# Kernel optimization log

Hardware: AMD Instinct MI355X
Metric: run time of the kernel (lower is better)

Reference implementation:

```python
import jax, jax.numpy as jnp
import numpy as np

N_NODES = 50000
IN_F, HID_F, OUT_F = 256, 128, 40
N_EDGES = 800000


def _uniform(key, shape, scale):
    return jax.random.uniform(key, shape, dtype=jnp.float32, minval=-scale, maxval=scale)


def setup_inputs() -> dict:
    key = jax.random.key(0)
    ks = jax.random.split(key, 20)
    x = jax.random.normal(ks[0], (N_NODES, IN_F), dtype=jnp.float32)
    edge_index = jax.random.randint(ks[1], (2, N_EDGES), 0, N_NODES, dtype=jnp.int64)
    s0, sa0 = 1.0 / np.sqrt(HID_F), 1.0  # std_att = 1/sqrt(1)
    s1, sa1 = 1.0 / np.sqrt(OUT_F), 1.0
    sv = 1.0 / np.sqrt(3.0)
    return {
        "x": x, "edge_index": edge_index,
        "Wl0": _uniform(ks[2], (IN_F, HID_F), s0),
        "Wh0": _uniform(ks[3], (IN_F, HID_F), s0),
        "Wm0": _uniform(ks[4], (IN_F, HID_F), s0),
        "al0": _uniform(ks[5], (HID_F, 1), sa0),
        "ah0": _uniform(ks[6], (HID_F, 1), sa0),
        "am0": _uniform(ks[7], (HID_F, 1), sa0),
        "att0": _uniform(ks[8], (3, 3), sv),
        "Wl1": _uniform(ks[9], (HID_F, OUT_F), s1),
        "Wh1": _uniform(ks[10], (HID_F, OUT_F), s1),
        "Wm1": _uniform(ks[11], (HID_F, OUT_F), s1),
        "al1": _uniform(ks[12], (OUT_F, 1), sa1),
        "ah1": _uniform(ks[13], (OUT_F, 1), sa1),
        "am1": _uniform(ks[14], (OUT_F, 1), sa1),
        "att1": _uniform(ks[15], (3, 3), sv),
    }


def _acm_layer(x, row, col, d_inv, Wl, Wh, Wm, al, ah, am, att):
    n = x.shape[0]
    hl, hh, hm = x @ Wl, x @ Wh, x @ Wm
    # adj_low @ M  with adj_low = D^{-1}(I + A): gather sources, scatter-add to rows
    def low(M):
        return d_inv[:, None] * (M + jax.ops.segment_sum(M[col], row, num_segments=n))
    out_low = jax.nn.relu(low(hl))
    out_high = jax.nn.relu(hh - low(hh))  # adj_high = I - adj_low
    out_mlp = jax.nn.relu(hm)
    T = 3.0
    sig = jax.nn.sigmoid(jnp.concatenate([out_low @ al, out_high @ ah, out_mlp @ am], axis=1))  # [n,3]
    a = jax.nn.softmax((sig @ att) / T, axis=1)
    return 3.0 * (a[:, 0:1] * out_low + a[:, 1:2] * out_high + a[:, 2:3] * out_mlp)


def reference(x, edge_index, Wl0, Wh0, Wm0, al0, ah0, am0, att0,
              Wl1, Wh1, Wm1, al1, ah1, am1, att1):
    n = x.shape[0]
    row, col = edge_index[0], edge_index[1]
    deg = jax.ops.segment_sum(jnp.ones_like(row, dtype=jnp.float32), row, num_segments=n)
    rowsum = 1.0 + deg  # rowsum of I + A (duplicates counted, as in scipy)
    d_inv = jnp.where(rowsum > 0, 1.0 / rowsum, 0.0)
    h = _acm_layer(x, row, col, d_inv, Wl0, Wh0, Wm0, al0, ah0, am0, att0)
    out = _acm_layer(h, row, col, d_inv, Wl1, Wh1, Wm1, al1, ah1, am1, att1)
    return out
```

## Files before the change

kernel.cpp:

```cpp
#include <hip/hip_runtime.h>
#include <math.h>

#define N_NODES 50000
#define N_EDGES 800000
#define IN_F    256
#define HID_F   128
#define OUT_F   40
#define W0N     (3*HID_F)
#define W1N     (3*OUT_F)
#define NB      ((N_NODES + 255) / 256)

#define XB   6250
#define P0B  ((IN_F * W0N) / 256)
#define P1B  ((HID_F * W1N) / 256)
#define CB0  (XB + P0B + P1B)
#define CNTB ((N_EDGES + 255) / 256)
#define PREPB (CB0 + CNTB)

typedef __attribute__((ext_vector_type(8))) unsigned short ushort8;
typedef __attribute__((ext_vector_type(4))) unsigned short ushort4v;
typedef __attribute__((ext_vector_type(8))) __bf16 bf16x8;
typedef __attribute__((ext_vector_type(4))) float f32x4;
typedef __attribute__((ext_vector_type(2))) float f32x2;

static __device__ __forceinline__ float sigmoidf_(float x) {
    return 1.0f / (1.0f + expf(-x));
}

static __device__ __forceinline__ unsigned short f2bf(float f) {
    unsigned u = __float_as_uint(f);
    u += 0x7FFFu + ((u >> 16) & 1u);
    return (unsigned short)(u >> 16);
}

static __device__ __forceinline__ float bflo(unsigned u) { return __uint_as_float(u << 16); }
static __device__ __forceinline__ float bfhi(unsigned u) { return __uint_as_float(u & 0xffff0000u); }


__global__ __launch_bounds__(256) void k_prep(
        const float* __restrict__ x, unsigned short* __restrict__ xb,
        const float* __restrict__ Wl0, const float* __restrict__ Wh0,
        const float* __restrict__ Wm0, unsigned short* __restrict__ W0t,
        const float* __restrict__ Wl1, const float* __restrict__ Wh1,
        const float* __restrict__ Wm1, unsigned short* __restrict__ W1t,
        const int* __restrict__ ei, int* __restrict__ deg) {
    int b = blockIdx.x, t = threadIdx.x;
    if (b < XB) {
        size_t idx = (size_t)b * 2048 + t * 8;
        float4 f0 = *(const float4*)(x + idx);
        float4 f1 = *(const float4*)(x + idx + 4);
        ushort8 u;
        u[0]=f2bf(f0.x); u[1]=f2bf(f0.y); u[2]=f2bf(f0.z); u[3]=f2bf(f0.w);
        u[4]=f2bf(f1.x); u[5]=f2bf(f1.y); u[6]=f2bf(f1.z); u[7]=f2bf(f1.w);
        *(ushort8*)(xb + idx) = u;
    } else if (b < XB + P0B) {
        int i = (b - XB) * 256 + t;
        int n = i / IN_F, k = i % IN_F;
        float v;
        if (n < HID_F)            v = Wl0[k * HID_F + n];
        else if (n < 2 * HID_F)   v = Wh0[k * HID_F + (n - HID_F)];
        else                      v = Wm0[k * HID_F + (n - 2 * HID_F)];
        W0t[i] = f2bf(v);
    } else if (b < CB0) {
        int i = (b - XB - P0B) * 256 + t;
        int n = i / HID_F, kp = i % HID_F;
        int k = ((kp >> 6) << 6) + ((kp & 3) << 4) + ((kp >> 2) & 15);
        float v;
        if (n < OUT_F)            v = Wl1[k * OUT_F + n];
        else if (n < 2 * OUT_F)   v = Wh1[k * OUT_F + (n - OUT_F)];
        else                      v = Wm1[k * OUT_F + (n - 2 * OUT_F)];
        W1t[i] = f2bf(v);
    } else {
        int e = (b - CB0) * 256 + t;
        if (e < N_EDGES) atomicAdd(&deg[ei[e]], 1);
    }
}


__global__ void k_scan1(const int* __restrict__ deg, int* __restrict__ rowPtr,
                        int* __restrict__ blkTot, float* __restrict__ dinv) {
    __shared__ int s[256];
    int t = threadIdx.x;
    int gid = blockIdx.x * 256 + t;
    int v = (gid < N_NODES) ? deg[gid] : 0;
    if (gid < N_NODES) dinv[gid] = 1.0f / (1.0f + (float)v);
    s[t] = v; __syncthreads();
    for (int d = 1; d < 256; d <<= 1) {
        int x = (t >= d) ? s[t - d] : 0;
        __syncthreads();
        s[t] += x;
        __syncthreads();
    }
    if (gid < N_NODES) rowPtr[gid] = s[t];
    if (t == 255) blkTot[blockIdx.x] = s[255];
}

__global__ void k_scan2(int* __restrict__ blk) {
    __shared__ int s[256];
    int t = threadIdx.x;
    int v = (t < NB) ? blk[t] : 0;
    s[t] = v; __syncthreads();
    for (int d = 1; d < 256; d <<= 1) {
        int x = (t >= d) ? s[t - d] : 0;
        __syncthreads();
        s[t] += x;
        __syncthreads();
    }
    if (t < NB) blk[t] = s[t] - v;
}

__global__ void k_scan3(const int* __restrict__ deg, const int* __restrict__ blkOff,
                        int* __restrict__ rowPtr) {
    int t = threadIdx.x;
    int gid = blockIdx.x * 256 + t;
    if (gid < N_NODES) rowPtr[gid] += blkOff[blockIdx.x] - deg[gid];
    if (gid == 0) rowPtr[N_NODES] = N_EDGES;
}


#define BKP 40

template<int EPI>
__global__ __launch_bounds__(256) void k_gemm_fill(
        const unsigned short* __restrict__ A, const unsigned short* __restrict__ Bt,
        unsigned short* __restrict__ C0, int ld0,
        unsigned short* __restrict__ C1, int ld1, int nsplit,
        unsigned short* __restrict__ Hs, unsigned char* __restrict__ Hq,
        unsigned short* __restrict__ HmP,
        int M, int N, int K, int nxt,
        const int* __restrict__ ei, const int* __restrict__ rowPtr,
        int* __restrict__ cursor, int* __restrict__ colIdx) {
    __shared__ unsigned short As[128 * BKP];
    __shared__ unsigned short Bs[128 * BKP];
    int tid  = threadIdx.x;

    if ((int)blockIdx.x >= nxt) {
        int fid = (blockIdx.x - nxt) * gridDim.y + blockIdx.y;
        int e = fid * 256 + tid;
        if (e < N_EDGES) {
            int r = ei[e];
            int c = ei[N_EDGES + e];
            int pos = rowPtr[r] + atomicAdd(&cursor[r], 1);
            colIdx[pos] = c;
        }
        return;
    }

    int lane = tid & 63, wid = tid >> 6;
    int wr = wid >> 1, wc = wid & 1;
    int bm = blockIdx.y * 128, bn = blockIdx.x * 128;

    int srow = tid >> 1;
    int scol = (tid & 1) * 16;

    int garow = min(bm + srow, M - 1);
    int gbrow = min(bn + srow, N - 1);

    f32x4 acc[4][4];
#pragma unroll
    for (int m = 0; m < 4; ++m)
#pragma unroll
        for (int n = 0; n < 4; ++n)
            acc[m][n] = (f32x4)(0.0f);

    int kg = (lane >> 4) * 8;
    int rA = wr * 64 + (lane & 15);
    int rB = wc * 64 + (lane & 15);

    for (int k0 = 0; k0 < K; k0 += 32) {
        {
            const unsigned short* src = A + (size_t)garow * K + k0 + scol;
            *(ushort8*)&As[srow * BKP + scol]     = *(const ushort8*)(src);
            *(ushort8*)&As[srow * BKP + scol + 8] = *(const ushort8*)(src + 8);
        }
        {
            const unsigned short* src = Bt + (size_t)gbrow * K + k0 + scol;
            *(ushort8*)&Bs[srow * BKP + scol]     = *(const ushort8*)(src);
            *(ushort8*)&Bs[srow * BKP + scol + 8] = *(const ushort8*)(src + 8);
        }
        __syncthreads();

        bf16x8 a[4], b[4];
#pragma unroll
        for (int m = 0; m < 4; ++m)
            a[m] = __builtin_bit_cast(bf16x8, *(const ushort8*)&As[(rA + m * 16) * BKP + kg]);
#pragma unroll
        for (int n = 0; n < 4; ++n)
            b[n] = __builtin_bit_cast(bf16x8, *(const ushort8*)&Bs[(rB + n * 16) * BKP + kg]);
#pragma unroll
        for (int m = 0; m < 4; ++m)
#pragma unroll
            for (int n = 0; n < 4; ++n)
                acc[m][n] = __builtin_amdgcn_mfma_f32_16x16x32_bf16(a[m], b[n], acc[m][n], 0, 0, 0);
        __syncthreads();
    }

    int col  = lane & 15;
    int rsub = (lane >> 4) * 4;

    if (EPI == 0) {
#pragma unroll
        for (int m = 0; m < 4; ++m) {
            int gm0 = bm + wr * 64 + m * 16 + rsub;
#pragma unroll
            for (int n = 0; n < 4; ++n) {
                int gn = bn + wc * 64 + n * 16 + col;
                if (gn >= N) continue;
#pragma unroll
                for (int j = 0; j < 4; ++j) {
                    int gm = gm0 + j;
                    if (gm >= M) continue;
                    unsigned short b = f2bf(acc[m][n][j]);
                    if (gn < nsplit) C0[(size_t)gm * ld0 + gn] = b;
                    else             C1[(size_t)gm * ld1 + (gn - nsplit)] = b;
                }
            }
        }
    } else {
#pragma unroll
        for (int m = 0; m < 4; ++m) {
            int gm0 = bm + wr * 64 + m * 16 + rsub;
#pragma unroll
            for (int j = 0; j < 4; ++j) {
                int gm = gm0 + j;
                if (gm >= M) continue;
                float v0 = acc[m][0][j], v1 = acc[m][1][j];
                float v2 = acc[m][2][j], v3 = acc[m][3][j];
                ushort4v o;
                o[0] = f2bf(v0); o[1] = f2bf(v1); o[2] = f2bf(v2); o[3] = f2bf(v3);
                if (bn < 256) {
                    int pos = bn + wc * 64 + col * 4;
                    *(ushort4v*)&Hs[(size_t)gm * 256 + pos] = o;
                    int pk = 0;
                    pk = __builtin_amdgcn_cvt_pk_fp8_f32(v0, v1, pk, false);
                    pk = __builtin_amdgcn_cvt_pk_fp8_f32(v2, v3, pk, true);
                    *(unsigned*)&Hq[(size_t)gm * 256 + pos] = (unsigned)pk;
                } else {
                    int pos = wc * 64 + col * 4;
                    *(ushort4v*)&HmP[(size_t)gm * 128 + pos] = o;
                }
            }
        }
    }
}


__global__ __launch_bounds__(256) void k_layer0(
        const unsigned short* __restrict__ Hs, const unsigned char* __restrict__ Hq,
        const unsigned short* __restrict__ HmP,
        const int* __restrict__ rowPtr, const int* __restrict__ colIdx,
        const float* __restrict__ dinv,
        const float* __restrict__ al, const float* __restrict__ ah,
        const float* __restrict__ am, const float* __restrict__ att,
        unsigned short* __restrict__ hout) {
    int lane = threadIdx.x & 63;
    int i = blockIdx.x * 4 + (threadIdx.x >> 6);

    int p0 = rowPtr[i], p1 = rowPtr[i + 1];
    float a0 = 0.f, a1 = 0.f, a2 = 0.f, a3 = 0.f;
    int off4 = lane * 4;
    int p = p0;
    for (; p + 7 < p1; p += 8) {
        int j[8];
#pragma unroll
        for (int q = 0; q < 8; ++q) j[q] = colIdx[p + q];
        unsigned w[8];
#pragma unroll
        for (int q = 0; q < 8; ++q) w[q] = *(const unsigned*)(Hq + (size_t)j[q] * 256 + off4);
#pragma unroll
        for (int q = 0; q < 8; ++q) {
            f32x2 d0 = __builtin_amdgcn_cvt_pk_f32_fp8((int)w[q], false);
            f32x2 d1 = __builtin_amdgcn_cvt_pk_f32_fp8((int)w[q], true);
            a0 += d0.x; a1 += d0.y; a2 += d1.x; a3 += d1.y;
        }
    }
    for (; p < p1; ++p) {
        int j = colIdx[p];
        unsigned w = *(const unsigned*)(Hq + (size_t)j * 256 + off4);
        f32x2 d0 = __builtin_amdgcn_cvt_pk_f32_fp8((int)w, false);
        f32x2 d1 = __builtin_amdgcn_cvt_pk_f32_fp8((int)w, true);
        a0 += d0.x; a1 += d0.y; a2 += d1.x; a3 += d1.y;
    }

    uint2 sv = *(const uint2*)(Hs + (size_t)i * 256 + off4);
    float s0 = bflo(sv.x), s1 = bfhi(sv.x), s2 = bflo(sv.y), s3 = bfhi(sv.y);
    float di = dinv[i];
    float l0 = di * (s0 + a0), l1 = di * (s1 + a1);
    float l2 = di * (s2 + a2), l3 = di * (s3 + a3);

    float ol0 = fmaxf(l0, 0.f), ol1 = fmaxf(l1, 0.f);
    float ol2 = fmaxf(l2, 0.f), ol3 = fmaxf(l3, 0.f);
    float oh0 = fmaxf(s0 - l0, 0.f), oh1 = fmaxf(s1 - l1, 0.f);
    float oh2 = fmaxf(s2 - l2, 0.f), oh3 = fmaxf(s3 - l3, 0.f);

    int c0 = ((lane >> 4) << 6) + (lane & 15);

    float om0 = 0.f, om1 = 0.f, om2 = 0.f, om3 = 0.f;
    float prA, prM = 0.f;
    if (lane < 32) {
        uint2 hv = *(const uint2*)(HmP + (size_t)i * 128 + off4);
        om0 = fmaxf(bflo(hv.x), 0.f); om1 = fmaxf(bfhi(hv.x), 0.f);
        om2 = fmaxf(bflo(hv.y), 0.f); om3 = fmaxf(bfhi(hv.y), 0.f);
        prA = ol0 * al[c0] + ol1 * al[c0 + 16] + ol2 * al[c0 + 32] + ol3 * al[c0 + 48];
        prM = om0 * am[c0] + om1 * am[c0 + 16] + om2 * am[c0 + 32] + om3 * am[c0 + 48];
    } else {
        int ch = c0 - 128;
        prA = oh0 * ah[ch] + oh1 * ah[ch + 16] + oh2 * ah[ch + 32] + oh3 * ah[ch + 48];
    }

#pragma unroll
    for (int d = 1; d < 32; d <<= 1) prA += __shfl_xor(prA, d);
#pragma unroll
    for (int d = 1; d < 32; d <<= 1) prM += __shfl_xor(prM, d);
    float g0 = __shfl(prA, 0);
    float g1 = __shfl(prA, 32);
    float g2 = __shfl(prM, 0);

    float sg0 = sigmoidf_(g0), sg1 = sigmoidf_(g1), sg2 = sigmoidf_(g2);
    const float inv3 = (1.0f / 3.0f);
    float e0 = (sg0 * att[0] + sg1 * att[3] + sg2 * att[6]) * inv3;
    float e1 = (sg0 * att[1] + sg1 * att[4] + sg2 * att[7]) * inv3;
    float e2 = (sg0 * att[2] + sg1 * att[5] + sg2 * att[8]) * inv3;
    float mx = fmaxf(e0, fmaxf(e1, e2));
    float x0 = expf(e0 - mx), x1 = expf(e1 - mx), x2 = expf(e2 - mx);
    float inv = 1.0f / (x0 + x1 + x2);
    float c0f = 3.0f * inv * x0, c1f = 3.0f * inv * x1, c2f = 3.0f * inv * x2;

    int src = lane | 32;
    float th0 = __shfl(oh0, src), th1 = __shfl(oh1, src);
    float th2 = __shfl(oh2, src), th3 = __shfl(oh3, src);

    if (lane < 32) {
        ushort4v o;
        o[0] = f2bf(c0f * ol0 + c1f * th0 + c2f * om0);
        o[1] = f2bf(c0f * ol1 + c1f * th1 + c2f * om1);
        o[2] = f2bf(c0f * ol2 + c1f * th2 + c2f * om2);
        o[3] = f2bf(c0f * ol3 + c1f * th3 + c2f * om3);
        *(ushort4v*)&hout[(size_t)i * 128 + off4] = o;
    }
}


__global__ __launch_bounds__(256) void k_layer1(
        const unsigned short* __restrict__ H1g, const unsigned short* __restrict__ H1m,
        const int* __restrict__ rowPtr, const int* __restrict__ colIdx,
        const float* __restrict__ dinv,
        const float* __restrict__ al, const float* __restrict__ ah,
        const float* __restrict__ am, const float* __restrict__ att,
        float* __restrict__ out) {
    int lane = threadIdx.x & 63;
    int i = blockIdx.x * 4 + (threadIdx.x >> 6);

    int p0 = rowPtr[i], p1 = rowPtr[i + 1];
    float a0 = 0.f, a1 = 0.f;
    int off = lane * 2;
    bool active = lane < 40;
    int p = p0;
    if (active) {
        for (; p + 7 < p1; p += 8) {
            int j[8];
#pragma unroll
            for (int q = 0; q < 8; ++q) j[q] = colIdx[p + q];
            unsigned v[8];
#pragma unroll
            for (int q = 0; q < 8; ++q) v[q] = *(const unsigned*)(H1g + (size_t)j[q] * 80 + off);
#pragma unroll
            for (int q = 0; q < 8; ++q) { a0 += bflo(v[q]); a1 += bfhi(v[q]); }
        }
        for (; p < p1; ++p) {
            int j = colIdx[p];
            unsigned v = *(const unsigned*)(H1g + (size_t)j * 80 + off);
            a0 += bflo(v); a1 += bfhi(v);
        }
    }

    float s0 = 0.f, s1 = 0.f;
    if (active) {
        unsigned sv = *(const unsigned*)(H1g + (size_t)i * 80 + off);
        s0 = bflo(sv); s1 = bfhi(sv);
    }
    float di = dinv[i];
    float l0 = di * (s0 + a0), l1 = di * (s1 + a1);

    float ol0 = fmaxf(l0, 0.f), ol1 = fmaxf(l1, 0.f);
    float oh0 = fmaxf(s0 - l0, 0.f), oh1 = fmaxf(s1 - l1, 0.f);

    float om0 = 0.f, om1 = 0.f;
    float r0 = 0.f, r1 = 0.f, r2 = 0.f;
    if (lane < 20) {
        unsigned hv = *(const unsigned*)(H1m + (size_t)i * 40 + off);
        om0 = fmaxf(bflo(hv), 0.f); om1 = fmaxf(bfhi(hv), 0.f);
        float2 alv = *(const float2*)(al + off);
        float2 amv = *(const float2*)(am + off);
        r0 = ol0 * alv.x + ol1 * alv.y;
        r2 = om0 * amv.x + om1 * amv.y;
    } else if (lane < 40) {
        float2 ahv = *(const float2*)(ah + (off - 40));
        r1 = oh0 * ahv.x + oh1 * ahv.y;
    }

#pragma unroll
    for (int d = 1; d < 64; d <<= 1) r0 += __shfl_xor(r0, d);
#pragma unroll
    for (int d = 1; d < 64; d <<= 1) r1 += __shfl_xor(r1, d);
#pragma unroll
    for (int d = 1; d < 64; d <<= 1) r2 += __shfl_xor(r2, d);

    float sg0 = sigmoidf_(r0), sg1 = sigmoidf_(r1), sg2 = sigmoidf_(r2);
    const float inv3 = (1.0f / 3.0f);
    float e0 = (sg0 * att[0] + sg1 * att[3] + sg2 * att[6]) * inv3;
    float e1 = (sg0 * att[1] + sg1 * att[4] + sg2 * att[7]) * inv3;
    float e2 = (sg0 * att[2] + sg1 * att[5] + sg2 * att[8]) * inv3;
    float mx = fmaxf(e0, fmaxf(e1, e2));
    float x0 = expf(e0 - mx), x1 = expf(e1 - mx), x2 = expf(e2 - mx);
    float inv = 1.0f / (x0 + x1 + x2);
    float c0 = 3.0f * inv * x0, c1 = 3.0f * inv * x1, c2 = 3.0f * inv * x2;

    int src = (lane + 20) & 63;
    float th0 = __shfl(oh0, src), th1 = __shfl(oh1, src);

    if (lane < 20) {
        float2 o;
        o.x = c0 * ol0 + c1 * th0 + c2 * om0;
        o.y = c0 * ol1 + c1 * th1 + c2 * om1;
        *(float2*)&out[(size_t)i * 40 + off] = o;
    }
}


extern "C" void kernel_launch(void* const* d_in, const int* in_sizes, int n_in,
                              void* d_out, int out_size, void* d_ws, size_t ws_size,
                              hipStream_t stream) {
    const float* x    = (const float*)d_in[0];
    const int*   ei   = (const int*)d_in[1];
    const float* Wl0  = (const float*)d_in[2];
    const float* Wh0  = (const float*)d_in[3];
    const float* Wm0  = (const float*)d_in[4];
    const float* al0  = (const float*)d_in[5];
    const float* ah0  = (const float*)d_in[6];
    const float* am0  = (const float*)d_in[7];
    const float* att0 = (const float*)d_in[8];
    const float* Wl1  = (const float*)d_in[9];
    const float* Wh1  = (const float*)d_in[10];
    const float* Wm1  = (const float*)d_in[11];
    const float* al1  = (const float*)d_in[12];
    const float* ah1  = (const float*)d_in[13];
    const float* am1  = (const float*)d_in[14];
    const float* att1 = (const float*)d_in[15];
    float* out = (float*)d_out;

    char* ws = (char*)d_ws;
    size_t off = 0;
    auto alloc = [&](size_t bytes) -> char* {
        char* p = ws + off;
        off += (bytes + 255) & ~(size_t)255;
        return p;
    };
    int*   degcur = (int*)  alloc((size_t)2 * N_NODES * 4);
    int*   deg    = degcur;
    int*   cursor = degcur + N_NODES;
    int*   rowPtr = (int*)  alloc((size_t)(N_NODES + 1) * 4);
    int*   colIdx = (int*)  alloc((size_t)N_EDGES * 4);
    int*   blkTot = (int*)  alloc(256 * 4);
    float* dinv   = (float*)alloc((size_t)N_NODES * 4);
    unsigned short* W0t  = (unsigned short*)alloc((size_t)W0N * IN_F * 2);
    unsigned short* W1t  = (unsigned short*)alloc((size_t)W1N * HID_F * 2);
    unsigned short* xb   = (unsigned short*)alloc((size_t)N_NODES * IN_F * 2);
    unsigned short* Hs   = (unsigned short*)alloc((size_t)N_NODES * 256 * 2);
    unsigned char*  Hq   = (unsigned char*) alloc((size_t)N_NODES * 256);
    unsigned short* HmP  = (unsigned short*)alloc((size_t)N_NODES * 128 * 2);
    unsigned short* H1g  = (unsigned short*)alloc((size_t)N_NODES * 80 * 2);
    unsigned short* H1m  = (unsigned short*)alloc((size_t)N_NODES * 40 * 2);
    unsigned short* hbuf = (unsigned short*)alloc((size_t)N_NODES * HID_F * 2);

    hipMemsetAsync(degcur, 0, (size_t)2 * N_NODES * 4, stream);
    k_prep<<<PREPB, 256, 0, stream>>>(x, xb, Wl0, Wh0, Wm0, W0t,
                                      Wl1, Wh1, Wm1, W1t, ei, deg);
    k_scan1<<<NB, 256, 0, stream>>>(deg, rowPtr, blkTot, dinv);
    k_scan2<<<1, 256, 0, stream>>>(blkTot);
    k_scan3<<<NB, 256, 0, stream>>>(deg, blkTot, rowPtr);
    {
        dim3 grid(3 + 8, (N_NODES + 127) / 128);
        k_gemm_fill<1><<<grid, 256, 0, stream>>>(xb, W0t,
                                                 nullptr, 0, nullptr, 0, 0,
                                                 Hs, Hq, HmP,
                                                 N_NODES, W0N, IN_F, 3,
                                                 ei, rowPtr, cursor, colIdx);
    }
    k_layer0<<<N_NODES / 4, 256, 0, stream>>>(Hs, Hq, HmP, rowPtr, colIdx, dinv,
                                              al0, ah0, am0, att0, hbuf);
    {
        dim3 grid(1, (N_NODES + 127) / 128);
        k_gemm_fill<0><<<grid, 256, 0, stream>>>(hbuf, W1t,
                                                 H1g, 80, H1m, 40, 80,
                                                 nullptr, nullptr, nullptr,
                                                 N_NODES, W1N, HID_F, 1,
                                                 nullptr, nullptr, nullptr, nullptr);
    }
    k_layer1<<<N_NODES / 4, 256, 0, stream>>>(H1g, H1m, rowPtr, colIdx, dinv,
                                              al1, ah1, am1, att1, out);
}
```

Before: 221.4 us.

## Record edge rank during degree count, single-block scan, and 16-bit CSR indices

The degree-count pass now saves each edge's atomic rank and a packed (row,col) word. The CSR fill can then place edges without a second atomic pass, and the cursor buffer is dropped. The three-kernel scan becomes one 1024-thread block that scans 49 nodes per thread serially, which removes two launches but the serial loops may be slow. Column indices are stored as 16-bit values to halve index traffic in the aggregation kernels, but 16 bits cannot hold node ids up to 50000 alongside the row in the packed 32-bit word... actually 50000 fits in 16 bits, so the packing is valid for this size.

```diff
diff --git a/kernel.cpp b/kernel.cpp
--- a/kernel.cpp
+++ b/kernel.cpp
@@ -8,7 +8,6 @@
 #define OUT_F   40
 #define W0N     (3*HID_F)
 #define W1N     (3*OUT_F)
-#define NB      ((N_NODES + 255) / 256)
 
 #define XB   6250
 #define P0B  ((IN_F * W0N) / 256)
@@ -43,7 +42,8 @@
         const float* __restrict__ Wm0, unsigned short* __restrict__ W0t,
         const float* __restrict__ Wl1, const float* __restrict__ Wh1,
         const float* __restrict__ Wm1, unsigned short* __restrict__ W1t,
-        const int* __restrict__ ei, int* __restrict__ deg) {
+        const int* __restrict__ ei, int* __restrict__ deg,
+        unsigned short* __restrict__ rank, unsigned* __restrict__ rc) {
     int b = blockIdx.x, t = threadIdx.x;
     if (b < XB) {
         size_t idx = (size_t)b * 2048 + t * 8;
@@ -72,49 +72,45 @@
         W1t[i] = f2bf(v);
     } else {
         int e = (b - CB0) * 256 + t;
-        if (e < N_EDGES) atomicAdd(&deg[ei[e]], 1);
-    }
-}
-
-
-__global__ void k_scan1(const int* __restrict__ deg, int* __restrict__ rowPtr,
-                        int* __restrict__ blkTot, float* __restrict__ dinv) {
-    __shared__ int s[256];
+        if (e < N_EDGES) {
+            int r = ei[e];
+            int c = ei[N_EDGES + e];
+            int old = atomicAdd(&deg[r], 1);
+            rank[e] = (unsigned short)old;
+            rc[e] = ((unsigned)r << 16) | (unsigned)c;
+        }
+    }
+}
+
+
+#define SCH 49
+
+__global__ __launch_bounds__(1024) void k_scan_all(
+        const int* __restrict__ deg, int* __restrict__ rowPtr,
+        float* __restrict__ dinv) {
+    __shared__ int s[1024];
     int t = threadIdx.x;
-    int gid = blockIdx.x * 256 + t;
-    int v = (gid < N_NODES) ? deg[gid] : 0;
-    if (gid < N_NODES) dinv[gid] = 1.0f / (1.0f + (float)v);
-    s[t] = v; __syncthreads();
-    for (int d = 1; d < 256; d <<= 1) {
+    int start = t * SCH;
+    int end = min(start + SCH, N_NODES);
+    int sum = 0;
+    for (int g = start; g < end; ++g) {
+        int v = deg[g];
+        dinv[g] = 1.0f / (1.0f + (float)v);
+        sum += v;
+    }
+    s[t] = sum; __syncthreads();
+    for (int d = 1; d < 1024; d <<= 1) {
         int x = (t >= d) ? s[t - d] : 0;
         __syncthreads();
         s[t] += x;
         __syncthreads();
     }
-    if (gid < N_NODES) rowPtr[gid] = s[t];
-    if (t == 255) blkTot[blockIdx.x] = s[255];
-}
-
-__global__ void k_scan2(int* __restrict__ blk) {
-    __shared__ int s[256];
-    int t = threadIdx.x;
-    int v = (t < NB) ? blk[t] : 0;
-    s[t] = v; __syncthreads();
-    for (int d = 1; d < 256; d <<= 1) {
-        int x = (t >= d) ? s[t - d] : 0;
-        __syncthreads();
-        s[t] += x;
-        __syncthreads();
-    }
-    if (t < NB) blk[t] = s[t] - v;
-}
-
-__global__ void k_scan3(const int* __restrict__ deg, const int* __restrict__ blkOff,
-                        int* __restrict__ rowPtr) {
-    int t = threadIdx.x;
-    int gid = blockIdx.x * 256 + t;
-    if (gid < N_NODES) rowPtr[gid] += blkOff[blockIdx.x] - deg[gid];
-    if (gid == 0) rowPtr[N_NODES] = N_EDGES;
+    int base = s[t] - sum;
+    for (int g = start; g < end; ++g) {
+        rowPtr[g] = base;
+        base += deg[g];
+    }
+    if (t == 1023) rowPtr[N_NODES] = N_EDGES;
 }
 
 
@@ -128,8 +124,8 @@
         unsigned short* __restrict__ Hs, unsigned char* __restrict__ Hq,
         unsigned short* __restrict__ HmP,
         int M, int N, int K, int nxt,
-        const int* __restrict__ ei, const int* __restrict__ rowPtr,
-        int* __restrict__ cursor, int* __restrict__ colIdx) {
+        const unsigned* __restrict__ rc, const unsigned short* __restrict__ rank,
+        const int* __restrict__ rowPtr, unsigned short* __restrict__ colIdx) {
     __shared__ unsigned short As[128 * BKP];
     __shared__ unsigned short Bs[128 * BKP];
     int tid  = threadIdx.x;
@@ -138,10 +134,10 @@
         int fid = (blockIdx.x - nxt) * gridDim.y + blockIdx.y;
         int e = fid * 256 + tid;
         if (e < N_EDGES) {
-            int r = ei[e];
-            int c = ei[N_EDGES + e];
-            int pos = rowPtr[r] + atomicAdd(&cursor[r], 1);
-            colIdx[pos] = c;
+            unsigned x = rc[e];
+            int r = (int)(x >> 16);
+            int pos = rowPtr[r] + (int)rank[e];
+            colIdx[pos] = (unsigned short)(x & 0xffffu);
         }
         return;
     }
@@ -248,7 +244,7 @@
 __global__ __launch_bounds__(256) void k_layer0(
         const unsigned short* __restrict__ Hs, const unsigned char* __restrict__ Hq,
         const unsigned short* __restrict__ HmP,
-        const int* __restrict__ rowPtr, const int* __restrict__ colIdx,
+        const int* __restrict__ rowPtr, const unsigned short* __restrict__ colIdx,
         const float* __restrict__ dinv,
         const float* __restrict__ al, const float* __restrict__ ah,
         const float* __restrict__ am, const float* __restrict__ att,
@@ -263,7 +259,7 @@
     for (; p + 7 < p1; p += 8) {
         int j[8];
 #pragma unroll
-        for (int q = 0; q < 8; ++q) j[q] = colIdx[p + q];
+        for (int q = 0; q < 8; ++q) j[q] = (int)colIdx[p + q];
         unsigned w[8];
 #pragma unroll
         for (int q = 0; q < 8; ++q) w[q] = *(const unsigned*)(Hq + (size_t)j[q] * 256 + off4);
@@ -275,7 +271,7 @@
         }
     }
     for (; p < p1; ++p) {
-        int j = colIdx[p];
+        int j = (int)colIdx[p];
         unsigned w = *(const unsigned*)(Hq + (size_t)j * 256 + off4);
         f32x2 d0 = __builtin_amdgcn_cvt_pk_f32_fp8((int)w, false);
         f32x2 d1 = __builtin_amdgcn_cvt_pk_f32_fp8((int)w, true);
@@ -343,7 +339,7 @@
 
 __global__ __launch_bounds__(256) void k_layer1(
         const unsigned short* __restrict__ H1g, const unsigned short* __restrict__ H1m,
-        const int* __restrict__ rowPtr, const int* __restrict__ colIdx,
+        const int* __restrict__ rowPtr, const unsigned short* __restrict__ colIdx,
         const float* __restrict__ dinv,
         const float* __restrict__ al, const float* __restrict__ ah,
         const float* __restrict__ am, const float* __restrict__ att,
@@ -360,7 +356,7 @@
         for (; p + 7 < p1; p += 8) {
             int j[8];
 #pragma unroll
-            for (int q = 0; q < 8; ++q) j[q] = colIdx[p + q];
+            for (int q = 0; q < 8; ++q) j[q] = (int)colIdx[p + q];
             unsigned v[8];
 #pragma unroll
             for (int q = 0; q < 8; ++q) v[q] = *(const unsigned*)(H1g + (size_t)j[q] * 80 + off);
@@ -368,7 +364,7 @@
             for (int q = 0; q < 8; ++q) { a0 += bflo(v[q]); a1 += bfhi(v[q]); }
         }
         for (; p < p1; ++p) {
-            int j = colIdx[p];
+            int j = (int)colIdx[p];
             unsigned v = *(const unsigned*)(H1g + (size_t)j * 80 + off);
             a0 += bflo(v); a1 += bfhi(v);
         }
@@ -456,12 +452,11 @@
         off += (bytes + 255) & ~(size_t)255;
         return p;
     };
-    int*   degcur = (int*)  alloc((size_t)2 * N_NODES * 4);
-    int*   deg    = degcur;
-    int*   cursor = degcur + N_NODES;
+    int*   deg    = (int*)  alloc((size_t)N_NODES * 4);
     int*   rowPtr = (int*)  alloc((size_t)(N_NODES + 1) * 4);
-    int*   colIdx = (int*)  alloc((size_t)N_EDGES * 4);
-    int*   blkTot = (int*)  alloc(256 * 4);
+    unsigned short* rank   = (unsigned short*)alloc((size_t)N_EDGES * 2);
+    unsigned*       rc     = (unsigned*)      alloc((size_t)N_EDGES * 4);
+    unsigned short* colIdx = (unsigned short*)alloc((size_t)N_EDGES * 2);
     float* dinv   = (float*)alloc((size_t)N_NODES * 4);
     unsigned short* W0t  = (unsigned short*)alloc((size_t)W0N * IN_F * 2);
     unsigned short* W1t  = (unsigned short*)alloc((size_t)W1N * HID_F * 2);
@@ -473,19 +468,17 @@
     unsigned short* H1m  = (unsigned short*)alloc((size_t)N_NODES * 40 * 2);
     unsigned short* hbuf = (unsigned short*)alloc((size_t)N_NODES * HID_F * 2);
 
-    hipMemsetAsync(degcur, 0, (size_t)2 * N_NODES * 4, stream);
+    hipMemsetAsync(deg, 0, (size_t)N_NODES * 4, stream);
     k_prep<<<PREPB, 256, 0, stream>>>(x, xb, Wl0, Wh0, Wm0, W0t,
-                                      Wl1, Wh1, Wm1, W1t, ei, deg);
-    k_scan1<<<NB, 256, 0, stream>>>(deg, rowPtr, blkTot, dinv);
-    k_scan2<<<1, 256, 0, stream>>>(blkTot);
-    k_scan3<<<NB, 256, 0, stream>>>(deg, blkTot, rowPtr);
+                                      Wl1, Wh1, Wm1, W1t, ei, deg, rank, rc);
+    k_scan_all<<<1, 1024, 0, stream>>>(deg, rowPtr, dinv);
     {
         dim3 grid(3 + 8, (N_NODES + 127) / 128);
         k_gemm_fill<1><<<grid, 256, 0, stream>>>(xb, W0t,
                                                  nullptr, 0, nullptr, 0, 0,
                                                  Hs, Hq, HmP,
                                                  N_NODES, W0N, IN_F, 3,
-                                                 ei, rowPtr, cursor, colIdx);
+                                                 rc, rank, rowPtr, colIdx);
     }
     k_layer0<<<N_NODES / 4, 256, 0, stream>>>(Hs, Hq, HmP, rowPtr, colIdx, dinv,
                                               al0, ah0, am0, att0, hbuf);
```

Result: slower. 298.8 us (+35.0%).

## Capture edge rank from degree atomic and store CSR column indices as 16-bit

Applied to the files above, without the earlier changes.

The degree-counting pass now saves each edge's slot (the old value returned by the atomic) plus a packed row/col word. The CSR fill step then places edges directly, with no second atomic pass over a cursor array. Column indices are stored as unsigned short, which halves index traffic in both aggregation kernels. The cost is extra rank and packed-edge buffers written in the prep kernel, and the layout relies on node count and per-row degree fitting in 16 bits.

```diff
diff --git a/kernel.cpp b/kernel.cpp
--- a/kernel.cpp
+++ b/kernel.cpp
@@ -43,7 +43,8 @@
         const float* __restrict__ Wm0, unsigned short* __restrict__ W0t,
         const float* __restrict__ Wl1, const float* __restrict__ Wh1,
         const float* __restrict__ Wm1, unsigned short* __restrict__ W1t,
-        const int* __restrict__ ei, int* __restrict__ deg) {
+        const int* __restrict__ ei, int* __restrict__ deg,
+        unsigned short* __restrict__ rank, unsigned* __restrict__ rc) {
     int b = blockIdx.x, t = threadIdx.x;
     if (b < XB) {
         size_t idx = (size_t)b * 2048 + t * 8;
@@ -72,7 +73,13 @@
         W1t[i] = f2bf(v);
     } else {
         int e = (b - CB0) * 256 + t;
-        if (e < N_EDGES) atomicAdd(&deg[ei[e]], 1);
+        if (e < N_EDGES) {
+            int r = ei[e];
+            int c = ei[N_EDGES + e];
+            int old = atomicAdd(&deg[r], 1);
+            rank[e] = (unsigned short)old;
+            rc[e] = ((unsigned)r << 16) | (unsigned)c;
+        }
     }
 }
 
@@ -128,8 +135,8 @@
         unsigned short* __restrict__ Hs, unsigned char* __restrict__ Hq,
         unsigned short* __restrict__ HmP,
         int M, int N, int K, int nxt,
-        const int* __restrict__ ei, const int* __restrict__ rowPtr,
-        int* __restrict__ cursor, int* __restrict__ colIdx) {
+        const unsigned* __restrict__ rc, const unsigned short* __restrict__ rank,
+        const int* __restrict__ rowPtr, unsigned short* __restrict__ colIdx) {
     __shared__ unsigned short As[128 * BKP];
     __shared__ unsigned short Bs[128 * BKP];
     int tid  = threadIdx.x;
@@ -138,10 +145,10 @@
         int fid = (blockIdx.x - nxt) * gridDim.y + blockIdx.y;
         int e = fid * 256 + tid;
         if (e < N_EDGES) {
-            int r = ei[e];
-            int c = ei[N_EDGES + e];
-            int pos = rowPtr[r] + atomicAdd(&cursor[r], 1);
-            colIdx[pos] = c;
+            unsigned x = rc[e];
+            int r = (int)(x >> 16);
+            int pos = rowPtr[r] + (int)rank[e];
+            colIdx[pos] = (unsigned short)(x & 0xffffu);
         }
         return;
     }
@@ -248,7 +255,7 @@
 __global__ __launch_bounds__(256) void k_layer0(
         const unsigned short* __restrict__ Hs, const unsigned char* __restrict__ Hq,
         const unsigned short* __restrict__ HmP,
-        const int* __restrict__ rowPtr, const int* __restrict__ colIdx,
+        const int* __restrict__ rowPtr, const unsigned short* __restrict__ colIdx,
         const float* __restrict__ dinv,
         const float* __restrict__ al, const float* __restrict__ ah,
         const float* __restrict__ am, const float* __restrict__ att,
@@ -263,7 +270,7 @@
     for (; p + 7 < p1; p += 8) {
         int j[8];
 #pragma unroll
-        for (int q = 0; q < 8; ++q) j[q] = colIdx[p + q];
+        for (int q = 0; q < 8; ++q) j[q] = (int)colIdx[p + q];
         unsigned w[8];
 #pragma unroll
         for (int q = 0; q < 8; ++q) w[q] = *(const unsigned*)(Hq + (size_t)j[q] * 256 + off4);
@@ -275,7 +282,7 @@
         }
     }
     for (; p < p1; ++p) {
-        int j = colIdx[p];
+        int j = (int)colIdx[p];
         unsigned w = *(const unsigned*)(Hq + (size_t)j * 256 + off4);
         f32x2 d0 = __builtin_amdgcn_cvt_pk_f32_fp8((int)w, false);
         f32x2 d1 = __builtin_amdgcn_cvt_pk_f32_fp8((int)w, true);
@@ -343,7 +350,7 @@
 
 __global__ __launch_bounds__(256) void k_layer1(
         const unsigned short* __restrict__ H1g, const unsigned short* __restrict__ H1m,
-        const int* __restrict__ rowPtr, const int* __restrict__ colIdx,
+        const int* __restrict__ rowPtr, const unsigned short* __restrict__ colIdx,
         const float* __restrict__ dinv,
         const float* __restrict__ al, const float* __restrict__ ah,
         const float* __restrict__ am, const float* __restrict__ att,
@@ -360,7 +367,7 @@
         for (; p + 7 < p1; p += 8) {
             int j[8];
 #pragma unroll
-            for (int q = 0; q < 8; ++q) j[q] = colIdx[p + q];
+            for (int q = 0; q < 8; ++q) j[q] = (int)colIdx[p + q];
             unsigned v[8];
 #pragma unroll
             for (int q = 0; q < 8; ++q) v[q] = *(const unsigned*)(H1g + (size_t)j[q] * 80 + off);
@@ -368,7 +375,7 @@
             for (int q = 0; q < 8; ++q) { a0 += bflo(v[q]); a1 += bfhi(v[q]); }
         }
         for (; p < p1; ++p) {
-            int j = colIdx[p];
+            int j = (int)colIdx[p];
             unsigned v = *(const unsigned*)(H1g + (size_t)j * 80 + off);
             a0 += bflo(v); a1 += bfhi(v);
         }
@@ -456,12 +463,12 @@
         off += (bytes + 255) & ~(size_t)255;
         return p;
     };
-    int*   degcur = (int*)  alloc((size_t)2 * N_NODES * 4);
-    int*   deg    = degcur;
-    int*   cursor = degcur + N_NODES;
+    int*   deg    = (int*)  alloc((size_t)N_NODES * 4);
     int*   rowPtr = (int*)  alloc((size_t)(N_NODES + 1) * 4);
-    int*   colIdx = (int*)  alloc((size_t)N_EDGES * 4);
     int*   blkTot = (int*)  alloc(256 * 4);
+    unsigned short* rank   = (unsigned short*)alloc((size_t)N_EDGES * 2);
+    unsigned*       rc     = (unsigned*)      alloc((size_t)N_EDGES * 4);
+    unsigned short* colIdx = (unsigned short*)alloc((size_t)N_EDGES * 2);
     float* dinv   = (float*)alloc((size_t)N_NODES * 4);
     unsigned short* W0t  = (unsigned short*)alloc((size_t)W0N * IN_F * 2);
     unsigned short* W1t  = (unsigned short*)alloc((size_t)W1N * HID_F * 2);
@@ -473,9 +480,9 @@
     unsigned short* H1m  = (unsigned short*)alloc((size_t)N_NODES * 40 * 2);
     unsigned short* hbuf = (unsigned short*)alloc((size_t)N_NODES * HID_F * 2);
 
-    hipMemsetAsync(degcur, 0, (size_t)2 * N_NODES * 4, stream);
+    hipMemsetAsync(deg, 0, (size_t)N_NODES * 4, stream);
     k_prep<<<PREPB, 256, 0, stream>>>(x, xb, Wl0, Wh0, Wm0, W0t,
-                                      Wl1, Wh1, Wm1, W1t, ei, deg);
+                                      Wl1, Wh1, Wm1, W1t, ei, deg, rank, rc);
     k_scan1<<<NB, 256, 0, stream>>>(deg, rowPtr, blkTot, dinv);
     k_scan2<<<1, 256, 0, stream>>>(blkTot);
     k_scan3<<<NB, 256, 0, stream>>>(deg, blkTot, rowPtr);
@@ -485,7 +492,7 @@
                                                  nullptr, 0, nullptr, 0, 0,
                                                  Hs, Hq, HmP,
                                                  N_NODES, W0N, IN_F, 3,
-                                                 ei, rowPtr, cursor, colIdx);
+                                                 rc, rank, rowPtr, colIdx);
     }
     k_layer0<<<N_NODES / 4, 256, 0, stream>>>(Hs, Hq, HmP, rowPtr, colIdx, dinv,
                                               al0, ah0, am0, att0, hbuf);
```

Measured after the change: 213.5 us. -3.6%, faster.
